# Kernel tuning notes

Hardware: AMD Instinct MI355X
Metric: run time of the kernel (lower is better)

Reference implementation:

```python
import jax, jax.numpy as jnp
import numpy as np

H = 60  # HIDDEN_SIZE
F = 1   # FEATURES


def gru_cell(x, h, wih, whh, bih, bhh):
    # torch GRU/GRUCell math: gates ordered [r, z, n]
    gi = x @ wih.T + bih
    gh = h @ whh.T + bhh
    i_r, i_z, i_n = jnp.split(gi, 3, axis=-1)
    h_r, h_z, h_n = jnp.split(gh, 3, axis=-1)
    r = jax.nn.sigmoid(i_r + h_r)
    z = jax.nn.sigmoid(i_z + h_z)
    n = jnp.tanh(i_n + r * h_n)
    return (1.0 - z) * n + z * h


def setup_inputs() -> dict:
    key = jax.random.key(0)
    ks = jax.random.split(key, 40)
    B, S_IN, S_OUT = 2048, 512, 512
    d = {}
    d["inputs"] = jax.random.normal(ks[0], (B, S_IN, F), jnp.float32)
    d["outputs"] = jax.random.normal(ks[1], (B, S_OUT, F), jnp.float32)

    def p(k, shape):
        return jax.random.normal(k, shape, jnp.float32) * 0.1

    i = 2
    # 3-layer encoder GRU (layer0 input dim F, others H)
    for l, din in enumerate([F, H, H]):
        d[f"enc_wih{l}"] = p(ks[i], (3 * H, din)); i += 1
        d[f"enc_whh{l}"] = p(ks[i], (3 * H, H)); i += 1
        d[f"enc_bih{l}"] = p(ks[i], (3 * H,)); i += 1
        d[f"enc_bhh{l}"] = p(ks[i], (3 * H,)); i += 1
    # 3 decoder GRUCells (cell1 input dim F, cells 2/3 input dim H)
    for c, din in zip([1, 2, 3], [F, H, H]):
        d[f"c{c}_wih"] = p(ks[i], (3 * H, din)); i += 1
        d[f"c{c}_whh"] = p(ks[i], (3 * H, H)); i += 1
        d[f"c{c}_bih"] = p(ks[i], (3 * H,)); i += 1
        d[f"c{c}_bhh"] = p(ks[i], (3 * H,)); i += 1
    d["lin_w"] = p(ks[i], (F, H)); i += 1
    d["lin_b"] = p(ks[i], (F,))
    return d


def reference(inputs, outputs,
              enc_wih0, enc_whh0, enc_bih0, enc_bhh0,
              enc_wih1, enc_whh1, enc_bih1, enc_bhh1,
              enc_wih2, enc_whh2, enc_bih2, enc_bhh2,
              c1_wih, c1_whh, c1_bih, c1_bhh,
              c2_wih, c2_whh, c2_bih, c2_bhh,
              c3_wih, c3_whh, c3_bih, c3_bhh,
              lin_w, lin_b):
    B = inputs.shape[0]
    xs = jnp.transpose(inputs, (1, 0, 2))  # [S_in, B, F] time-major for scan
    enc_params = [
        (enc_wih0, enc_whh0, enc_bih0, enc_bhh0),
        (enc_wih1, enc_whh1, enc_bih1, enc_bhh1),
        (enc_wih2, enc_whh2, enc_bih2, enc_bhh2),
    ]
    # Encoder: stacked 3-layer GRU; dropout between layers is identity (eval mode)
    h_final = []
    layer_in = xs
    for wih, whh, bih, bhh in enc_params:
        h0 = jnp.zeros((B, H), inputs.dtype)

        def step(h, x, wih=wih, whh=whh, bih=bih, bhh=bhh):
            hn = gru_cell(x, h, wih, whh, bih, bhh)
            return hn, hn

        hT, ys = jax.lax.scan(step, h0, layer_in)
        h_final.append(hT)
        layer_in = ys
    # original: ht1 = encoded_vec[2] (top layer), ht2 = [1], ht3 = [0]
    ht1, ht2, ht3 = h_final[2], h_final[1], h_final[0]

    dec_xs = jnp.transpose(outputs, (1, 0, 2))  # [S_out, B, F]

    def dstep(carry, x):
        h1, h2, h3 = carry
        h1 = gru_cell(x, h1, c1_wih, c1_whh, c1_bih, c1_bhh)
        h2 = gru_cell(h1, h2, c2_wih, c2_whh, c2_bih, c2_bhh)  # dropout(h1) = identity
        h3 = gru_cell(h2, h3, c3_wih, c3_whh, c3_bih, c3_bhh)
        y = h3 @ lin_w.T + lin_b
        return (h1, h2, h3), y

    _, ys = jax.lax.scan(dstep, (ht1, ht2, ht3), dec_xs)  # ys: [S_out, B, F]
    return jnp.transpose(ys, (1, 0, 2))  # [B, S_out, F]
```

## Files before the change

### kernel.cpp

```cpp
#include <hip/hip_runtime.h>
#include <hip/hip_bf16.h>


typedef float    f32x4 __attribute__((ext_vector_type(4)));
typedef _Float16 f16x8 __attribute__((ext_vector_type(8)));

#define RSTR 72
#define REG  (16 * RSTR)

struct CellB  { const float* bih; const float* bhh; const float* wih_vec; };
struct PhaseArgs {
  const float* xseq;
  const unsigned short* frags;
  CellB cell[3];
  const float* hfin_rd;
  float* hfin_wr;
  const float* lin_b;
  float* y;
};
struct PrepArgs {
  const float* w[13];
  int din[13];
  unsigned short* out;
};

union HU { _Float16 h; unsigned short u; };
__device__ __forceinline__ unsigned short f2h(float x) { HU c; c.h = (_Float16)x; return c.u; }
__device__ __forceinline__ float h2f(unsigned short s) { HU c; c.u = s; return (float)c.h; }
__device__ __forceinline__ void wg_barrier() {
  asm volatile("s_waitcnt lgkmcnt(0)" ::: "memory");
  __builtin_amdgcn_s_barrier();
}

__global__ void prep_frags(PrepArgs P) {
  int id = blockIdx.x * 256 + threadIdx.x;
  int e    = id & 7;
  int lane = (id >> 3) & 63;
  int sp   = (id >> 9) & 1;
  int s2   = (id >> 10) & 1;
  int rest = id >> 11;
  int tile = rest % 12;
  int cm   = rest / 12;
  if (cm > 12) return;
  const float* W = P.w[cm];
  int din = P.din[cm];
  int c = tile * 16 + (lane & 15);
  int k = s2 * 32 + (lane >> 4) * 8 + e;
  float v = 0.f;
  if (cm == 12) {
    if (c == 0 && k < 60) v = W[k];
  } else {
    int j = c & 63, sec = c >> 6;
    if (j < 60 && k < din) v = W[(sec * 60 + j) * din + k];
  }
  unsigned short hi = f2h(v);
  unsigned short o = sp ? f2h(v - h2f(hi)) : hi;
  P.out[id] = o;
}

__device__ __forceinline__ f32x4 mmh(f32x4 acc, const f16x8 A[2], const f16x8 B[2][2]) {
  f32x4 a2 = {0.f, 0.f, 0.f, 0.f};
  acc = __builtin_amdgcn_mfma_f32_16x16x32_f16(A[0], B[0][0], acc, 0, 0, 0);
  a2  = __builtin_amdgcn_mfma_f32_16x16x32_f16(A[0], B[0][1], a2,  0, 0, 0);
  acc = __builtin_amdgcn_mfma_f32_16x16x32_f16(A[1], B[1][0], acc, 0, 0, 0);
  a2  = __builtin_amdgcn_mfma_f32_16x16x32_f16(A[1], B[1][1], a2,  0, 0, 0);
  return acc + a2;
}
__device__ __forceinline__ f32x4 mmx(f32x4 acc, const f16x8 A[2], const f16x8 B[2]) {
  acc = __builtin_amdgcn_mfma_f32_16x16x32_f16(A[0], B[0], acc, 0, 0, 0);
  acc = __builtin_amdgcn_mfma_f32_16x16x32_f16(A[1], B[1], acc, 0, 0, 0);
  return acc;
}

template <int IS_DEC>
__global__ __launch_bounds__(768, 3) void gru_phase(PhaseArgs P) {
  __shared__ alignas(16) unsigned short ring[6 * REG];

  const int tid  = threadIdx.x;
  const int lane = tid & 63;
  const int wid  = tid >> 6;
  const int g    = wid >> 2;
  const int w    = wid & 3;
  const int c16  = lane & 15;
  const int q16  = lane >> 4;
  const int row_base = blockIdx.x * 16;
  const int c    = w * 16 + c16;
  const bool cv  = (c < 60);
  const int cell = (IS_DEC ? 3 : 0) + g;
  const bool din1 = (g == 0);
  const bool yduty = (IS_DEC && g == 0 && w == 0);

  int wo[4];
#pragma unroll
  for (int q = 0; q < 4; ++q) wo[q] = (4 * q16 + q) * RSTR + c;
  const int ro0 = c16 * RSTR + q16 * 8;
  const int ro1 = ro0 + 32;

  const float* bih = P.cell[g].bih;
  const float* bhh = P.cell[g].bhh;
  float b_r  = cv ? bih[c] + bhh[c]           : 0.f;
  float b_z  = cv ? bih[60 + c] + bhh[60 + c] : 0.f;
  float b_hn = cv ? bhh[120 + c]              : 0.f;
  float b_in = cv ? bih[120 + c]              : 0.f;
  float w_r = 0.f, w_z = 0.f, w_n = 0.f;
  if (din1 && cv) {
    const float* wv = P.cell[g].wih_vec;
    w_r = wv[c]; w_z = wv[60 + c]; w_n = wv[120 + c];
  }

  f16x8 Bh[3][2][2], Bx[3][2];
#pragma unroll
  for (int T = 0; T < 3; ++T)
#pragma unroll
    for (int s2 = 0; s2 < 2; ++s2) {
      const int tile = w + 4 * T;
#pragma unroll
      for (int sp = 0; sp < 2; ++sp)
        Bh[T][s2][sp] = *(const f16x8*)(P.frags +
            (size_t)(((cell * 2 + 1) * 12 + tile) * 4 + s2 * 2 + sp) * 512 + lane * 8);
      Bx[T][s2] = *(const f16x8*)(P.frags +
          (size_t)(((cell * 2 + 0) * 12 + tile) * 4 + s2 * 2 + 0) * 512 + lane * 8);
    }
  f16x8 Lw[2][2];
  float lb = 0.f;
  if (IS_DEC) {
    lb = P.lin_b[0];
#pragma unroll
    for (int s2 = 0; s2 < 2; ++s2)
#pragma unroll
      for (int sp = 0; sp < 2; ++sp)
        Lw[s2][sp] = *(const f16x8*)(P.frags +
            (size_t)((12 * 12 + 0) * 4 + s2 * 2 + sp) * 512 + lane * 8);
  }

  float hreg[4];
#pragma unroll
  for (int q = 0; q < 4; ++q) {
    float h0 = 0.f;
    if (IS_DEC && cv)
      h0 = P.hfin_rd[((size_t)(2 - g) * 2048 + row_base + 4 * q16 + q) * 64 + c];
    hreg[q] = h0;
    ring[(g * 2 + 1) * REG + wo[q]] = f2h(h0);
  }

  float xcur[4] = {0.f, 0.f, 0.f, 0.f};
  if (din1) {
    const float* xp = P.xseq + (size_t)row_base * 512;
#pragma unroll
    for (int q = 0; q < 4; ++q) xcur[q] = xp[(size_t)(4 * q16 + q) * 512];
  }
  wg_barrier();

#pragma unroll 1
  for (int s = 0; s < 514; ++s) {
    if (yduty && s >= 3) {
      const int yb = (4 + ((s + 1) & 1)) * REG;
      f16x8 Yh[2];
      Yh[0] = *(const f16x8*)(ring + yb + ro0);
      Yh[1] = *(const f16x8*)(ring + yb + ro1);
      f32x4 ya = {lb, lb, lb, lb};
      ya = mmh(ya, Yh, Lw);
      if (c16 == 0) {
#pragma unroll
        for (int q = 0; q < 4; ++q)
          P.y[(size_t)(row_base + 4 * q16 + q) * 512 + (s - 3)] = ya[q];
      }
    }

    const int t = s - g;
    if (t >= 0 && t < 512) {
      const int oR = (g * 2 + ((t + 1) & 1)) * REG;
      f16x8 Ah[2];
      Ah[0] = *(const f16x8*)(ring + oR + ro0);
      Ah[1] = *(const f16x8*)(ring + oR + ro1);
      f16x8 Xh[2];
      if (!din1) {
        const int oX = ((g - 1) * 2 + (t & 1)) * REG;
        Xh[0] = *(const f16x8*)(ring + oX + ro0);
        Xh[1] = *(const f16x8*)(ring + oX + ro1);
      }

      f32x4 aR  = {b_r, b_r, b_r, b_r};
      f32x4 aZ  = {b_z, b_z, b_z, b_z};
      f32x4 aHN = {b_hn, b_hn, b_hn, b_hn};
      f32x4 aIN = {b_in, b_in, b_in, b_in};
      aR  = mmh(aR,  Ah, Bh[0]);
      aZ  = mmh(aZ,  Ah, Bh[1]);
      aHN = mmh(aHN, Ah, Bh[2]);

      if (din1) {
#pragma unroll
        for (int q = 0; q < 4; ++q) {
          aR[q]  += xcur[q] * w_r;
          aZ[q]  += xcur[q] * w_z;
          aIN[q] += xcur[q] * w_n;
        }
        if (t + 1 < 512) {
          const float* xp = P.xseq + (size_t)row_base * 512 + (t + 1);
#pragma unroll
          for (int q = 0; q < 4; ++q) xcur[q] = xp[(size_t)(4 * q16 + q) * 512];
        }
      } else {
        aR  = mmx(aR,  Xh, Bx[0]);
        aZ  = mmx(aZ,  Xh, Bx[1]);
        aIN = mmx(aIN, Xh, Bx[2]);
      }

      unsigned short* wp = ring + (g * 2 + (t & 1)) * REG;
#pragma unroll
      for (int q = 0; q < 4; ++q) {
        float r = __builtin_amdgcn_rcpf(1.f + __expf(-aR[q]));
        float z = __builtin_amdgcn_rcpf(1.f + __expf(-aZ[q]));
        float na = aIN[q] + r * aHN[q];
        float e2 = __expf(2.f * na);
        float n  = __builtin_fmaf(-2.f, __builtin_amdgcn_rcpf(e2 + 1.f), 1.f);
        float h  = n + z * (hreg[q] - n);
        hreg[q]  = h;
        wp[wo[q]] = f2h(h);
      }

      if (!IS_DEC && t == 511) {
#pragma unroll
        for (int q = 0; q < 4; ++q)
          P.hfin_wr[((size_t)g * 2048 + row_base + 4 * q16 + q) * 64 + c] = hreg[q];
      }
    }
    wg_barrier();
  }

  if (yduty) {
    const int yb = 5 * REG;
    f16x8 Yh[2];
    Yh[0] = *(const f16x8*)(ring + yb + ro0);
    Yh[1] = *(const f16x8*)(ring + yb + ro1);
    f32x4 ya = {lb, lb, lb, lb};
    ya = mmh(ya, Yh, Lw);
    if (c16 == 0) {
#pragma unroll
      for (int q = 0; q < 4; ++q)
        P.y[(size_t)(row_base + 4 * q16 + q) * 512 + 511] = ya[q];
    }
  }
}

extern "C" void kernel_launch(void* const* d_in, const int* in_sizes, int n_in,
                              void* d_out, int out_size, void* d_ws, size_t ws_size,
                              hipStream_t stream) {
  (void)in_sizes; (void)n_in; (void)out_size; (void)ws_size;
  const float* inputs  = (const float*)d_in[0];
  const float* outputs = (const float*)d_in[1];

  unsigned short* frags = (unsigned short*)d_ws;
  float* hfin = (float*)((char*)d_ws + 655360);

  static const int ofs[6]  = {2, 6, 10, 14, 18, 22};
  static const int dins[6] = {1, 60, 60, 1, 60, 60};

  PrepArgs pa;
  for (int ci = 0; ci < 6; ++ci) {
    pa.w[ci * 2 + 0]   = (const float*)d_in[ofs[ci] + 0];
    pa.w[ci * 2 + 1]   = (const float*)d_in[ofs[ci] + 1];
    pa.din[ci * 2 + 0] = dins[ci];
    pa.din[ci * 2 + 1] = 60;
  }
  pa.w[12]   = (const float*)d_in[26];
  pa.din[12] = 60;
  pa.out = frags;
  prep_frags<<<dim3(1248), dim3(256), 0, stream>>>(pa);

  PhaseArgs ea;
  ea.xseq = inputs; ea.frags = frags;
  for (int gg = 0; gg < 3; ++gg) {
    ea.cell[gg].bih     = (const float*)d_in[ofs[gg] + 2];
    ea.cell[gg].bhh     = (const float*)d_in[ofs[gg] + 3];
    ea.cell[gg].wih_vec = (const float*)d_in[ofs[gg] + 0];
  }
  ea.hfin_rd = hfin; ea.hfin_wr = hfin;
  ea.lin_b = (const float*)d_in[27];
  ea.y = (float*)d_out;
  gru_phase<0><<<dim3(128), dim3(768), 0, stream>>>(ea);

  PhaseArgs da = ea;
  da.xseq = outputs;
  for (int gg = 0; gg < 3; ++gg) {
    da.cell[gg].bih     = (const float*)d_in[ofs[3 + gg] + 2];
    da.cell[gg].bhh     = (const float*)d_in[ofs[3 + gg] + 3];
    da.cell[gg].wih_vec = (const float*)d_in[ofs[3 + gg] + 0];
  }
  gru_phase<1><<<dim3(128), dim3(768), 0, stream>>>(da);
}
```

Before: 1.169 ms.

## Process two 16-row sub-batches per workgroup, halving grid size

Each workgroup now handles 32 batch rows as two independent 16-row sub-blocks with separate LDS rings, and the grid is halved from 128 to 64 blocks. Interleaving two independent recurrences per step gives more MFMA and transcendental work between barriers and amortises barrier and latency costs across both sub-blocks. The output linear projection also drops the low-precision split term (mmh to mmx), which removes a few MFMAs but loses some accuracy. The trade-off is fewer blocks on a GPU with many CUs, so half as many CUs do the work while each does roughly twice as much per step.

After: 2.404 ms. +105.7%, slower.

```diff
diff --git a/kernel.cpp b/kernel.cpp
--- a/kernel.cpp
+++ b/kernel.cpp
@@ -7,6 +7,7 @@
 
 #define RSTR 72
 #define REG  (16 * RSTR)
+#define SUBSZ (6 * REG)
 
 struct CellB  { const float* bih; const float* bhh; const float* wih_vec; };
 struct PhaseArgs {
@@ -58,23 +59,25 @@
   P.out[id] = o;
 }
 
-__device__ __forceinline__ f32x4 mmh(f32x4 acc, const f16x8 A[2], const f16x8 B[2][2]) {
+__device__ __forceinline__ f32x4 mmh(f32x4 acc, const f16x8 A0, const f16x8 A1,
+                                     const f16x8 B[2][2]) {
   f32x4 a2 = {0.f, 0.f, 0.f, 0.f};
-  acc = __builtin_amdgcn_mfma_f32_16x16x32_f16(A[0], B[0][0], acc, 0, 0, 0);
-  a2  = __builtin_amdgcn_mfma_f32_16x16x32_f16(A[0], B[0][1], a2,  0, 0, 0);
-  acc = __builtin_amdgcn_mfma_f32_16x16x32_f16(A[1], B[1][0], acc, 0, 0, 0);
-  a2  = __builtin_amdgcn_mfma_f32_16x16x32_f16(A[1], B[1][1], a2,  0, 0, 0);
+  acc = __builtin_amdgcn_mfma_f32_16x16x32_f16(A0, B[0][0], acc, 0, 0, 0);
+  a2  = __builtin_amdgcn_mfma_f32_16x16x32_f16(A0, B[0][1], a2,  0, 0, 0);
+  acc = __builtin_amdgcn_mfma_f32_16x16x32_f16(A1, B[1][0], acc, 0, 0, 0);
+  a2  = __builtin_amdgcn_mfma_f32_16x16x32_f16(A1, B[1][1], a2,  0, 0, 0);
   return acc + a2;
 }
-__device__ __forceinline__ f32x4 mmx(f32x4 acc, const f16x8 A[2], const f16x8 B[2]) {
-  acc = __builtin_amdgcn_mfma_f32_16x16x32_f16(A[0], B[0], acc, 0, 0, 0);
-  acc = __builtin_amdgcn_mfma_f32_16x16x32_f16(A[1], B[1], acc, 0, 0, 0);
+__device__ __forceinline__ f32x4 mmx(f32x4 acc, const f16x8 A0, const f16x8 A1,
+                                     const f16x8 B[2]) {
+  acc = __builtin_amdgcn_mfma_f32_16x16x32_f16(A0, B[0], acc, 0, 0, 0);
+  acc = __builtin_amdgcn_mfma_f32_16x16x32_f16(A1, B[1], acc, 0, 0, 0);
   return acc;
 }
 
 template <int IS_DEC>
 __global__ __launch_bounds__(768, 3) void gru_phase(PhaseArgs P) {
-  __shared__ alignas(16) unsigned short ring[6 * REG];
+  __shared__ alignas(16) unsigned short ring[2 * SUBSZ];
 
   const int tid  = threadIdx.x;
   const int lane = tid & 63;
@@ -83,12 +86,13 @@
   const int w    = wid & 3;
   const int c16  = lane & 15;
   const int q16  = lane >> 4;
-  const int row_base = blockIdx.x * 16;
+  const int row_base = blockIdx.x * 32;
   const int c    = w * 16 + c16;
   const bool cv  = (c < 60);
   const int cell = (IS_DEC ? 3 : 0) + g;
   const bool din1 = (g == 0);
-  const bool yduty = (IS_DEC && g == 0 && w == 0);
+  const int  ysub  = w;
+  const bool yduty = (IS_DEC && g == 0 && w < 2);
 
   int wo[4];
 #pragma unroll
@@ -121,124 +125,129 @@
       Bx[T][s2] = *(const f16x8*)(P.frags +
           (size_t)(((cell * 2 + 0) * 12 + tile) * 4 + s2 * 2 + 0) * 512 + lane * 8);
     }
-  f16x8 Lw[2][2];
+  f16x8 Lw[2];
   float lb = 0.f;
   if (IS_DEC) {
     lb = P.lin_b[0];
 #pragma unroll
     for (int s2 = 0; s2 < 2; ++s2)
-#pragma unroll
-      for (int sp = 0; sp < 2; ++sp)
-        Lw[s2][sp] = *(const f16x8*)(P.frags +
-            (size_t)((12 * 12 + 0) * 4 + s2 * 2 + sp) * 512 + lane * 8);
-  }
-
-  float hreg[4];
-#pragma unroll
-  for (int q = 0; q < 4; ++q) {
-    float h0 = 0.f;
-    if (IS_DEC && cv)
-      h0 = P.hfin_rd[((size_t)(2 - g) * 2048 + row_base + 4 * q16 + q) * 64 + c];
-    hreg[q] = h0;
-    ring[(g * 2 + 1) * REG + wo[q]] = f2h(h0);
-  }
-
-  float xcur[4] = {0.f, 0.f, 0.f, 0.f};
+      Lw[s2] = *(const f16x8*)(P.frags +
+          (size_t)((12 * 12 + 0) * 4 + s2 * 2 + 0) * 512 + lane * 8);
+  }
+
+  float hreg[2][4];
+#pragma unroll
+  for (int sb = 0; sb < 2; ++sb)
+#pragma unroll
+    for (int q = 0; q < 4; ++q) {
+      float h0 = 0.f;
+      if (IS_DEC && cv)
+        h0 = P.hfin_rd[((size_t)(2 - g) * 2048 + row_base + sb * 16 + 4 * q16 + q) * 64 + c];
+      hreg[sb][q] = h0;
+      ring[sb * SUBSZ + (g * 2 + 1) * REG + wo[q]] = f2h(h0);
+    }
+
+  float xcur[2][4] = {};
   if (din1) {
-    const float* xp = P.xseq + (size_t)row_base * 512;
-#pragma unroll
-    for (int q = 0; q < 4; ++q) xcur[q] = xp[(size_t)(4 * q16 + q) * 512];
+#pragma unroll
+    for (int sb = 0; sb < 2; ++sb)
+#pragma unroll
+      for (int q = 0; q < 4; ++q)
+        xcur[sb][q] = P.xseq[(size_t)(row_base + sb * 16 + 4 * q16 + q) * 512];
   }
   wg_barrier();
 
 #pragma unroll 1
   for (int s = 0; s < 514; ++s) {
     if (yduty && s >= 3) {
-      const int yb = (4 + ((s + 1) & 1)) * REG;
-      f16x8 Yh[2];
-      Yh[0] = *(const f16x8*)(ring + yb + ro0);
-      Yh[1] = *(const f16x8*)(ring + yb + ro1);
+      const int yb = ysub * SUBSZ + (4 + ((s + 1) & 1)) * REG;
+      f16x8 Y0 = *(const f16x8*)(ring + yb + ro0);
+      f16x8 Y1 = *(const f16x8*)(ring + yb + ro1);
       f32x4 ya = {lb, lb, lb, lb};
-      ya = mmh(ya, Yh, Lw);
+      ya = mmx(ya, Y0, Y1, Lw);
       if (c16 == 0) {
 #pragma unroll
         for (int q = 0; q < 4; ++q)
-          P.y[(size_t)(row_base + 4 * q16 + q) * 512 + (s - 3)] = ya[q];
+          P.y[(size_t)(row_base + ysub * 16 + 4 * q16 + q) * 512 + (s - 3)] = ya[q];
       }
     }
 
     const int t = s - g;
     if (t >= 0 && t < 512) {
       const int oR = (g * 2 + ((t + 1) & 1)) * REG;
-      f16x8 Ah[2];
-      Ah[0] = *(const f16x8*)(ring + oR + ro0);
-      Ah[1] = *(const f16x8*)(ring + oR + ro1);
-      f16x8 Xh[2];
-      if (!din1) {
-        const int oX = ((g - 1) * 2 + (t & 1)) * REG;
-        Xh[0] = *(const f16x8*)(ring + oX + ro0);
-        Xh[1] = *(const f16x8*)(ring + oX + ro1);
+      const int oW = (g * 2 + (t & 1)) * REG;
+      const int oX = din1 ? 0 : ((g - 1) * 2 + (t & 1)) * REG;
+
+#pragma unroll
+      for (int sb = 0; sb < 2; ++sb) {
+        f16x8 A0 = *(const f16x8*)(ring + sb * SUBSZ + oR + ro0);
+        f16x8 A1 = *(const f16x8*)(ring + sb * SUBSZ + oR + ro1);
+        f16x8 X0, X1;
+        if (!din1) {
+          X0 = *(const f16x8*)(ring + sb * SUBSZ + oX + ro0);
+          X1 = *(const f16x8*)(ring + sb * SUBSZ + oX + ro1);
+        }
+
+        f32x4 aR  = {b_r, b_r, b_r, b_r};
+        f32x4 aZ  = {b_z, b_z, b_z, b_z};
+        f32x4 aHN = {b_hn, b_hn, b_hn, b_hn};
+        f32x4 aIN = {b_in, b_in, b_in, b_in};
+        aR  = mmh(aR,  A0, A1, Bh[0]);
+        aZ  = mmh(aZ,  A0, A1, Bh[1]);
+        aHN = mmh(aHN, A0, A1, Bh[2]);
+
+        if (din1) {
+#pragma unroll
+          for (int q = 0; q < 4; ++q) {
+            aR[q]  += xcur[sb][q] * w_r;
+            aZ[q]  += xcur[sb][q] * w_z;
+            aIN[q] += xcur[sb][q] * w_n;
+          }
+          if (t + 1 < 512) {
+            const float* xp = P.xseq + (size_t)(row_base + sb * 16) * 512 + (t + 1);
+#pragma unroll
+            for (int q = 0; q < 4; ++q) xcur[sb][q] = xp[(size_t)(4 * q16 + q) * 512];
+          }
+        } else {
+          aR  = mmx(aR,  X0, X1, Bx[0]);
+          aZ  = mmx(aZ,  X0, X1, Bx[1]);
+          aIN = mmx(aIN, X0, X1, Bx[2]);
+        }
+
+        unsigned short* wp = ring + sb * SUBSZ + oW;
+#pragma unroll
+        for (int q = 0; q < 4; ++q) {
+          float r = __builtin_amdgcn_rcpf(1.f + __expf(-aR[q]));
+          float z = __builtin_amdgcn_rcpf(1.f + __expf(-aZ[q]));
+          float na = aIN[q] + r * aHN[q];
+          float e2 = __expf(2.f * na);
+          float n  = __builtin_fmaf(-2.f, __builtin_amdgcn_rcpf(e2 + 1.f), 1.f);
+          float h  = n + z * (hreg[sb][q] - n);
+          hreg[sb][q] = h;
+          wp[wo[q]] = f2h(h);
+        }
+
+        if (!IS_DEC && t == 511) {
+#pragma unroll
+          for (int q = 0; q < 4; ++q)
+            P.hfin_wr[((size_t)g * 2048 + row_base + sb * 16 + 4 * q16 + q) * 64 + c] =
+                hreg[sb][q];
+        }
       }
-
-      f32x4 aR  = {b_r, b_r, b_r, b_r};
-      f32x4 aZ  = {b_z, b_z, b_z, b_z};
-      f32x4 aHN = {b_hn, b_hn, b_hn, b_hn};
-      f32x4 aIN = {b_in, b_in, b_in, b_in};
-      aR  = mmh(aR,  Ah, Bh[0]);
-      aZ  = mmh(aZ,  Ah, Bh[1]);
-      aHN = mmh(aHN, Ah, Bh[2]);
-
-      if (din1) {
-#pragma unroll
-        for (int q = 0; q < 4; ++q) {
-          aR[q]  += xcur[q] * w_r;
-          aZ[q]  += xcur[q] * w_z;
-          aIN[q] += xcur[q] * w_n;
-        }
-        if (t + 1 < 512) {
-          const float* xp = P.xseq + (size_t)row_base * 512 + (t + 1);
-#pragma unroll
-          for (int q = 0; q < 4; ++q) xcur[q] = xp[(size_t)(4 * q16 + q) * 512];
-        }
-      } else {
-        aR  = mmx(aR,  Xh, Bx[0]);
-        aZ  = mmx(aZ,  Xh, Bx[1]);
-        aIN = mmx(aIN, Xh, Bx[2]);
-      }
-
-      unsigned short* wp = ring + (g * 2 + (t & 1)) * REG;
-#pragma unroll
-      for (int q = 0; q < 4; ++q) {
-        float r = __builtin_amdgcn_rcpf(1.f + __expf(-aR[q]));
-        float z = __builtin_amdgcn_rcpf(1.f + __expf(-aZ[q]));
-        float na = aIN[q] + r * aHN[q];
-        float e2 = __expf(2.f * na);
-        float n  = __builtin_fmaf(-2.f, __builtin_amdgcn_rcpf(e2 + 1.f), 1.f);
-        float h  = n + z * (hreg[q] - n);
-        hreg[q]  = h;
-        wp[wo[q]] = f2h(h);
-      }
-
-      if (!IS_DEC && t == 511) {
-#pragma unroll
-        for (int q = 0; q < 4; ++q)
-          P.hfin_wr[((size_t)g * 2048 + row_base + 4 * q16 + q) * 64 + c] = hreg[q];
-      }
     }
     wg_barrier();
   }
 
   if (yduty) {
-    const int yb = 5 * REG;
-    f16x8 Yh[2];
-    Yh[0] = *(const f16x8*)(ring + yb + ro0);
-    Yh[1] = *(const f16x8*)(ring + yb + ro1);
+    const int yb = ysub * SUBSZ + 5 * REG;
+    f16x8 Y0 = *(const f16x8*)(ring + yb + ro0);
+    f16x8 Y1 = *(const f16x8*)(ring + yb + ro1);
     f32x4 ya = {lb, lb, lb, lb};
-    ya = mmh(ya, Yh, Lw);
+    ya = mmx(ya, Y0, Y1, Lw);
     if (c16 == 0) {
 #pragma unroll
       for (int q = 0; q < 4; ++q)
-        P.y[(size_t)(row_base + 4 * q16 + q) * 512 + 511] = ya[q];
+        P.y[(size_t)(row_base + ysub * 16 + 4 * q16 + q) * 512 + 511] = ya[q];
     }
   }
 }
@@ -278,7 +287,7 @@
   ea.hfin_rd = hfin; ea.hfin_wr = hfin;
   ea.lin_b = (const float*)d_in[27];
   ea.y = (float*)d_out;
-  gru_phase<0><<<dim3(128), dim3(768), 0, stream>>>(ea);
+  gru_phase<0><<<dim3(64), dim3(768), 0, stream>>>(ea);
 
   PhaseArgs da = ea;
   da.xseq = outputs;
@@ -287,5 +296,5 @@
     da.cell[gg].bhh     = (const float*)d_in[ofs[3 + gg] + 3];
     da.cell[gg].wih_vec = (const float*)d_in[ofs[3 + gg] + 0];
   }
-  gru_phase<1><<<dim3(128), dim3(768), 0, stream>>>(da);
-}
+  gru_phase<1><<<dim3(64), dim3(768), 0, stream>>>(da);
+}
```
